# Kernel optimization log

Hardware: AMD Instinct MI355X
Metric: run time of the kernel (lower is better)

## Reference

```python
import jax, jax.numpy as jnp
import numpy as np

NEG_INF = -jnp.inf


def setup_inputs() -> dict:
    key = jax.random.key(0)
    ks = jax.random.split(key, 20)
    B, N, M = 8, 1024, 128
    F_OP, F_MA, F_E, OUT, HID = 64, 64, 16, 64, 128
    inp = {
        "x": jax.random.normal(ks[0], (B, N, F_OP), dtype=jnp.float32),
        "y": jax.random.normal(ks[1], (B, M, F_MA), dtype=jnp.float32),
        "z": jax.random.normal(ks[2], (B, N, M, F_E), dtype=jnp.float32),
        "op_adj_in": jax.random.randint(ks[3], (B, N, N), 0, 2, dtype=jnp.int32),
        "ma_adj_in": jax.random.randint(ks[4], (B, N, N), 0, 2, dtype=jnp.int32),
        "op_ma_adj": jax.random.randint(ks[5], (B, N, M), 0, 2, dtype=jnp.int32),
        # learned parameters
        "weight_op": jax.random.normal(ks[6], (F_OP, OUT), dtype=jnp.float32) * 0.1,
        "weight_ma": jax.random.normal(ks[7], (F_MA, OUT), dtype=jnp.float32) * 0.1,
        "weight_edge": jax.random.normal(ks[8], (F_E, OUT), dtype=jnp.float32) * 0.1,
        "attention_op": jax.random.normal(ks[9], (1, 2 * OUT), dtype=jnp.float32) * 0.1,
        "attention_ma": jax.random.normal(ks[10], (1, 3 * OUT), dtype=jnp.float32) * 0.1,
        "w1": jax.random.normal(ks[11], (2 * OUT, HID), dtype=jnp.float32) * 0.1,
        "b1": jnp.zeros((HID,), dtype=jnp.float32),
        "w2": jax.random.normal(ks[12], (HID, HID), dtype=jnp.float32) * 0.1,
        "b2": jnp.zeros((HID,), dtype=jnp.float32),
        "wo": jax.random.normal(ks[13], (HID, OUT), dtype=jnp.float32) * 0.1,
        "bo": jnp.zeros((OUT,), dtype=jnp.float32),
    }
    return inp


def reference(x, y, z, op_adj_in, ma_adj_in, op_ma_adj,
              weight_op, weight_ma, weight_edge, attention_op, attention_ma,
              w1, b1, w2, b2, wo, bo):
    OUT = weight_op.shape[1]
    h = jnp.einsum('bni,io->bno', x, weight_op)  # [B,N,OUT]
    # all_combinations[b,i,j] = cat(h[b,j], h[b,i]); dot with attention_op splits:
    a1 = attention_op[0, :OUT]
    a2 = attention_op[0, OUT:]
    e_op = (h @ a2)[:, :, None] + (h @ a1)[:, None, :]  # [B,N,N]
    e_op = jax.nn.leaky_relu(e_op, negative_slope=0.01)

    adj = (jnp.swapaxes(op_adj_in, 1, 2) + op_adj_in
           + jnp.swapaxes(ma_adj_in, 1, 2) + ma_adj_in)  # [B,N,N]
    row_mask = jnp.all(op_ma_adj == 0, axis=-1)  # [B,N] ops with no machine link
    adj = jnp.where(row_mask[:, :, None], 1, adj)
    att = jnp.where(adj > 0, e_op, NEG_INF)
    attention_in_op = jax.nn.softmax(att, axis=2)
    h_prime_op = jnp.einsum('bij,bjo->bio', attention_in_op, h)  # [B,N,OUT]

    h_ma = jnp.einsum('bmi,io->bmo', y, weight_ma)  # [B,M,OUT]
    h_edge = jnp.einsum('bnmi,io->bnmo', z, weight_edge)  # [B,N,M,OUT]
    # cat([h_op_i, h_ma_j, h_edge_ij]) @ attention_ma split into three dots
    am1 = attention_ma[0, :OUT]
    am2 = attention_ma[0, OUT:2 * OUT]
    am3 = attention_ma[0, 2 * OUT:]
    e_ma = (h @ am1)[:, :, None] + (h_ma @ am2)[:, None, :] + h_edge @ am3  # [B,N,M]
    e_ma = jax.nn.leaky_relu(e_ma, negative_slope=0.01)

    adj2 = jnp.where(row_mask[:, :, None], 1, op_ma_adj)
    att2 = jnp.where(adj2 > 0, e_ma, NEG_INF)
    attention_in_ma = jax.nn.softmax(att2, axis=2)  # [B,N,M]
    h_ma_edge = h_ma[:, None, :, :] + h_edge  # [B,N,M,OUT]
    h_prime_ma = jnp.einsum('bnm,bnmo->bno', attention_in_ma, h_ma_edge) + h

    h_prime = jnp.concatenate([h_prime_op, h_prime_ma], axis=-1)  # [B,N,2*OUT]
    embed = jax.nn.elu(h_prime @ w1 + b1)
    embed = jax.nn.elu(embed @ w2 + b2)
    embed = embed @ wo + bo
    embed = jnp.where(row_mask[:, :, None], 0.0, embed)
    return embed
```

## Files before the change

kernel.cpp:

```cpp
#include <hip/hip_runtime.h>
#include <math.h>

#define BB 8
#define NN 1024
#define MM 128
#define FOUT 64
#define HIDN 128

#define OFF_H       0
#define OFF_HMA     524288
#define OFF_HA1     589824
#define OFF_HA2     598016
#define OFF_HAM1    606208
#define OFF_HMAAM2  614400
#define OFF_RMASK   615424
#define OFF_WAM3    623616
#define OFF_HPRIME  623632
#define OFF_RDIR    1672208
#define OFF_OPMB    1934352
#define OFF_WT1HI   1967120
#define OFF_WT1LO   1975312
#define OFF_WT2HI   1983504
#define OFF_WT2LO   1991696
#define OFF_WTOHI   1999888
#define OFF_WTOLO   2003984
#define OFF_HTHI    2008080
#define OFF_HTLO    2270224
#define OFF_HMATHI  2532368
#define OFF_HMATLO  2565136

typedef __attribute__((ext_vector_type(8))) short bf16x8;
typedef __attribute__((ext_vector_type(8))) unsigned short u16x8;
typedef __attribute__((ext_vector_type(4))) float f32x4;

__device__ __forceinline__ void splitbf(float v, unsigned short& h, unsigned short& l) {
    unsigned u = __float_as_uint(v);
    unsigned hb = (u + 0x7FFFu + ((u >> 16) & 1u)) >> 16;
    float hf = __uint_as_float(hb << 16);
    float lf = v - hf;
    unsigned ul = __float_as_uint(lf);
    unsigned lb = (ul + 0x7FFFu + ((ul >> 16) & 1u)) >> 16;
    h = (unsigned short)hb; l = (unsigned short)lb;
}

__global__ __launch_bounds__(256) void k1_prep(
    const float* __restrict__ x, const float* __restrict__ y,
    const int* __restrict__ op_ma_adj,
    const int* __restrict__ op_adj, const int* __restrict__ ma_adj,
    const float* __restrict__ w_op, const float* __restrict__ w_ma,
    const float* __restrict__ w_edge,
    const float* __restrict__ att_op, const float* __restrict__ att_ma,
    const float* __restrict__ w1_g, const float* __restrict__ w2_g,
    const float* __restrict__ wo_g,
    float* __restrict__ h, float* __restrict__ h_ma,
    float* __restrict__ ha1, float* __restrict__ ha2, float* __restrict__ ham1,
    float* __restrict__ hmaam2, int* __restrict__ rmask, float* __restrict__ wam3,
    unsigned long long* __restrict__ rowdir, unsigned long long* __restrict__ opmb,
    unsigned short* __restrict__ wt1hi, unsigned short* __restrict__ wt1lo,
    unsigned short* __restrict__ wt2hi, unsigned short* __restrict__ wt2lo,
    unsigned short* __restrict__ wtohi, unsigned short* __restrict__ wtolo,
    unsigned short* __restrict__ hthi, unsigned short* __restrict__ htlo,
    unsigned short* __restrict__ hmathi, unsigned short* __restrict__ hmatlo)
{
    __shared__ float wlds[64 * 64];
    __shared__ unsigned hstage[32 * 64];
    int bid = blockIdx.x;
    int t = threadIdx.x;
    int lane = t & 63;
    int wv = t >> 6;

    if (bid < 256) {
        int b = bid >> 5;
        int n0g = (bid & 31) * 32;
        for (int k = t; k < 4096; k += 256) wlds[k] = w_op[k];
        float a1c = att_op[lane], a2c = att_op[64 + lane], am1c = att_ma[lane];
        __syncthreads();
        #pragma unroll
        for (int p = 0; p < 8; ++p) {
            int row = b * NN + n0g + p * 4 + wv;
            float xv = x[(size_t)row * 64 + lane];
            float acc = 0.f;
            #pragma unroll
            for (int i = 0; i < 64; ++i) {
                float xi = __shfl(xv, i);
                acc += xi * wlds[i * 64 + lane];
            }
            h[(size_t)row * 64 + lane] = acc;
            unsigned short hs, ls;
            splitbf(acc, hs, ls);
            hstage[(p * 4 + wv) * 64 + lane] = (unsigned)hs | ((unsigned)ls << 16);
            float d1 = acc * a1c, d2 = acc * a2c, d3 = acc * am1c;
            #pragma unroll
            for (int m = 32; m; m >>= 1) {
                d1 += __shfl_xor(d1, m);
                d2 += __shfl_xor(d2, m);
                d3 += __shfl_xor(d3, m);
            }
            int v0 = op_ma_adj[(size_t)row * 128 + lane];
            int v1 = op_ma_adj[(size_t)row * 128 + 64 + lane];
            unsigned long long w0 = __ballot(v0 != 0);
            unsigned long long w1 = __ballot(v1 != 0);
            if (lane == 0) {
                ha1[row] = d1; ha2[row] = d2; ham1[row] = d3;
                opmb[row * 2] = w0; opmb[row * 2 + 1] = w1;
                rmask[row] = ((w0 | w1) == 0ULL) ? 1 : 0;
            }
        }
        __syncthreads();
        {
            int plane = t >> 7;
            int q = t & 127;
            int o = q >> 1;
            int hf = q & 1;
            int sh = plane * 16;
            unsigned short* dst = plane ? htlo : hthi;
            u16x8 pk0, pk1;
            #pragma unroll
            for (int k = 0; k < 8; ++k)
                pk0[k] = (unsigned short)((hstage[(hf * 16 + k) * 64 + o] >> sh) & 0xFFFFu);
            #pragma unroll
            for (int k = 0; k < 8; ++k)
                pk1[k] = (unsigned short)((hstage[(hf * 16 + 8 + k) * 64 + o] >> sh) & 0xFFFFu);
            size_t base = ((size_t)(b * 64 + o)) * 1024 + n0g + hf * 16;
            *(u16x8*)&dst[base] = pk0;
            *(u16x8*)&dst[base + 8] = pk1;
        }
    } else if (bid < 288) {
        int bb = (bid - 256) >> 2;
        int m0 = ((bid - 256) & 3) * 32;
        for (int k = t; k < 4096; k += 256) wlds[k] = w_ma[k];
        float am2c = att_ma[64 + lane];
        __syncthreads();
        #pragma unroll
        for (int p = 0; p < 8; ++p) {
            int row = bb * MM + m0 + p * 4 + wv;
            float yv = y[(size_t)row * 64 + lane];
            float acc = 0.f;
            #pragma unroll
            for (int i = 0; i < 64; ++i) {
                float yi = __shfl(yv, i);
                acc += yi * wlds[i * 64 + lane];
            }
            h_ma[(size_t)row * 64 + lane] = acc;
            unsigned short hs, ls;
            splitbf(acc, hs, ls);
            hstage[(p * 4 + wv) * 64 + lane] = (unsigned)hs | ((unsigned)ls << 16);
            float d = acc * am2c;
            #pragma unroll
            for (int m = 32; m; m >>= 1) d += __shfl_xor(d, m);
            if (lane == 0) hmaam2[row] = d;
        }
        __syncthreads();
        {
            int plane = t >> 7;
            int q = t & 127;
            int o = q >> 1;
            int hf = q & 1;
            int sh = plane * 16;
            unsigned short* dst = plane ? hmatlo : hmathi;
            u16x8 pk0, pk1;
            #pragma unroll
            for (int k = 0; k < 8; ++k)
                pk0[k] = (unsigned short)((hstage[(hf * 16 + k) * 64 + o] >> sh) & 0xFFFFu);
            #pragma unroll
            for (int k = 0; k < 8; ++k)
                pk1[k] = (unsigned short)((hstage[(hf * 16 + 8 + k) * 64 + o] >> sh) & 0xFFFFu);
            size_t base = ((size_t)(bb * 64 + o)) * 128 + m0 + hf * 16;
            *(u16x8*)&dst[base] = pk0;
            *(u16x8*)&dst[base + 8] = pk1;
        }
    } else if (bid == 288) {
        if (t < 16) {
            float s = 0.f;
            for (int o = 0; o < 64; ++o) s += w_edge[t * 64 + o] * att_ma[128 + o];
            wam3[t] = s;
        }
    } else if (bid < 2337) {
        unsigned char (*nib)[4][64] = (unsigned char(*)[4][64])wlds;
        int p = bid - 289;
        int b = p >> 8;
        int rg = p & 255;
        int rl = t >> 6;
        int row = rg * 4 + rl;
        const int4* oprow = (const int4*)(op_adj + ((size_t)(b * NN + row)) * NN);
        const int4* marow = (const int4*)(ma_adj + ((size_t)(b * NN + row)) * NN);
        #pragma unroll
        for (int p2 = 0; p2 < 4; ++p2) {
            int4 vo = oprow[p2 * 64 + lane];
            int4 vm = marow[p2 * 64 + lane];
            unsigned nb = ((vo.x | vm.x) ? 1u : 0u) | ((vo.y | vm.y) ? 2u : 0u)
                        | ((vo.z | vm.z) ? 4u : 0u) | ((vo.w | vm.w) ? 8u : 0u);
            nib[rl][p2][lane] = (unsigned char)nb;
        }
        __syncthreads();
        if (t < 64) {
            int arl = t >> 4, q = t & 15;
            const unsigned* nw = (const unsigned*)&nib[arl][q >> 2][(q & 3) * 16];
            unsigned long long w = 0;
            #pragma unroll
            for (int u = 0; u < 4; ++u) {
                unsigned v = nw[u];
                w |= (unsigned long long)(v & 0xFu)         << (16 * u);
                w |= (unsigned long long)((v >> 8) & 0xFu)  << (16 * u + 4);
                w |= (unsigned long long)((v >> 16) & 0xFu) << (16 * u + 8);
                w |= (unsigned long long)((v >> 24) & 0xFu) << (16 * u + 12);
            }
            rowdir[((size_t)(b * NN + rg * 4 + arl)) * 16 + q] = w;
        }
    } else {
        float (*tls)[33] = (float(*)[33])wlds;
        int p = bid - 2337;
        const float* src; unsigned short *dhi, *dlo; int KD, CD, tI, tJ;
        if (p < 16)      { src = w1_g; dhi = wt1hi; dlo = wt1lo; KD = 128; CD = 128; tI = p >> 2; tJ = p & 3; }
        else if (p < 32) { src = w2_g; dhi = wt2hi; dlo = wt2lo; KD = 128; CD = 128; tI = (p-16) >> 2; tJ = (p-16) & 3; }
        else             { src = wo_g; dhi = wtohi; dlo = wtolo; KD = 128; CD = 64;  tI = (p-32) >> 1; tJ = (p-32) & 1; }
        int k0 = tI * 32, c0 = tJ * 32;
        #pragma unroll
        for (int it = 0; it < 4; ++it) {
            int r = (t >> 5) + it * 8;
            int c = t & 31;
            tls[r][c] = src[(size_t)(k0 + r) * CD + c0 + c];
        }
        __syncthreads();
        #pragma unroll
        for (int it = 0; it < 4; ++it) {
            int c = (t >> 5) + it * 8;
            int k = t & 31;
            unsigned short hs, ls;
            splitbf(tls[k][c], hs, ls);
            dhi[(size_t)(c0 + c) * KD + k0 + k] = hs;
            dlo[(size_t)(c0 + c) * KD + k0 + k] = ls;
        }
    }
}

__global__ __launch_bounds__(256) void k2_opatt(
    const unsigned long long* __restrict__ rowdir,
    const unsigned short* __restrict__ hthi,
    const unsigned short* __restrict__ htlo,
    const float* __restrict__ ha1, const float* __restrict__ ha2,
    const int* __restrict__ rmask, float* __restrict__ h_prime)
{
    __shared__ __align__(16) unsigned short Pl[16 * 1024];
    __shared__ float ha1s[1024];
    __shared__ unsigned long long dirw[16][16];
    __shared__ unsigned short trw[1024];
    __shared__ float rdeninv[16];
    int bid = blockIdx.x;
    int b = bid >> 6;
    int i0 = (bid & 63) << 4;
    int t = threadIdx.x;

    {
        int row = t >> 4, w = t & 15;
        dirw[row][w] = rowdir[((size_t)(b * NN + i0 + row)) * 16 + w];
    }
    {
        const char* base = (const char*)rowdir + (size_t)b * NN * 128 + (i0 >> 3);
        #pragma unroll
        for (int jj = 0; jj < 4; ++jj) {
            int j = t + jj * 256;
            trw[j] = *(const unsigned short*)(base + (size_t)j * 128);
        }
    }
    ha1s[t] = ha1[b * NN + t];
    ha1s[t + 256] = ha1[b * NN + t + 256];
    ha1s[t + 512] = ha1[b * NN + t + 512];
    ha1s[t + 768] = ha1[b * NN + t + 768];
    __syncthreads();

    {
        int row = t >> 4, q = t & 15;
        int bn = b * NN + i0 + row;
        float ha2i = ha2[bn];
        unsigned rmf = rmask[bn] ? 1u : 0u;

        float mx = -INFINITY;
        #pragma unroll 8
        for (int jj = 0; jj < 64; ++jj) {
            int j = q + (jj << 4);
            float ev = ha2i + ha1s[j];
            ev = ev > 0.f ? ev : 0.01f * ev;
            unsigned bit = ((unsigned)(dirw[row][jj >> 2] >> (q + ((jj & 3) << 4))) & 1u)
                         | ((unsigned)(trw[j] >> row) & 1u) | rmf;
            if (bit) mx = fmaxf(mx, ev);
        }
        #pragma unroll
        for (int m = 1; m < 16; m <<= 1) mx = fmaxf(mx, __shfl_xor(mx, m));

        float s = 0.f;
        #pragma unroll 4
        for (int jj = 0; jj < 64; ++jj) {
            int j = q + (jj << 4);
            float ev = ha2i + ha1s[j];
            ev = ev > 0.f ? ev : 0.01f * ev;
            unsigned bit = ((unsigned)(dirw[row][jj >> 2] >> (q + ((jj & 3) << 4))) & 1u)
                         | ((unsigned)(trw[j] >> row) & 1u) | rmf;
            float u = bit ? __expf(ev - mx) : 0.f;
            s += u;
            unsigned ub = __float_as_uint(u);
            unsigned short pb = (unsigned short)((ub + 0x7FFFu + ((ub >> 16) & 1u)) >> 16);
            unsigned byteoff = ((unsigned)(row * 2048 + j * 2)) ^ ((unsigned)((row & 7) << 4));
            *(unsigned short*)((char*)Pl + byteoff) = pb;
        }
        #pragma unroll
        for (int m = 1; m < 16; m <<= 1) s += __shfl_xor(s, m);
        if (q == 0) rdeninv[row] = 1.f / s;
    }
    __syncthreads();

    {
        int lane = t & 63, wvv = t >> 6;
        int arow = lane & 15, kg = lane >> 4;
        int col = wvv * 16 + arow;
        const unsigned short* bhp = hthi + ((size_t)(b * 64 + col)) * 1024;
        const unsigned short* blp = htlo + ((size_t)(b * 64 + col)) * 1024;
        f32x4 acc = {0.f, 0.f, 0.f, 0.f};
        #pragma unroll 8
        for (int kst = 0; kst < 32; ++kst) {
            unsigned cc = ((unsigned)(kst * 4 + kg)) ^ ((unsigned)(arow & 7));
            bf16x8 pa = *(const bf16x8*)((char*)Pl + arow * 2048 + cc * 16);
            bf16x8 vh = *(const bf16x8*)&bhp[kst * 32 + kg * 8];
            bf16x8 vl = *(const bf16x8*)&blp[kst * 32 + kg * 8];
            acc = __builtin_amdgcn_mfma_f32_16x16x32_bf16(pa, vh, acc, 0, 0, 0);
            acc = __builtin_amdgcn_mfma_f32_16x16x32_bf16(pa, vl, acc, 0, 0, 0);
        }
        size_t base = (size_t)(b * NN + i0);
        #pragma unroll
        for (int r = 0; r < 4; ++r) {
            int orow = kg * 4 + r;
            float v = acc[r] * rdeninv[orow];
            h_prime[(base + orow) * 128 + col] = v;
        }
    }
}

__global__ __launch_bounds__(256) void k3_maatt(
    const float* __restrict__ z, const unsigned long long* __restrict__ opmb,
    const float* __restrict__ h,
    const unsigned short* __restrict__ hmathi, const unsigned short* __restrict__ hmatlo,
    const float* __restrict__ ham1, const float* __restrict__ hmaam2,
    const int* __restrict__ rmask, const float* __restrict__ wam3,
    const float* __restrict__ w_edge, float* __restrict__ h_prime)
{
    __shared__ __align__(16) unsigned short U_lds[16 * 136];
    __shared__ float wedge_s[1024];
    __shared__ float wam3s[16];
    __shared__ float zsum_s[16][16];
    __shared__ float zpart[4][16];
    __shared__ float redmx[4], redsm[4];
    __shared__ float rdeninv[16];

    int bid = blockIdx.x;
    int b = bid >> 6;
    int n0 = (bid & 63) * 16;
    int t = threadIdx.x;
    int lane = t & 63;
    int wvid = t >> 6;
    int ns = t >> 7;
    int m = t & 127;

    for (int k = t; k < 1024; k += 256) wedge_s[k] = w_edge[k];
    if (t < 16) wam3s[t] = wam3[t];
    __syncthreads();

    float hmam2v = hmaam2[b * MM + m];

    for (int pp = 0; pp < 8; ++pp) {
        int n = n0 + pp * 2 + ns;
        int bn = b * NN + n;

        float zv[16];
        {
            size_t zbase = ((size_t)bn * MM + m) * 16;
            float4 z0 = *(const float4*)(z + zbase);
            float4 z1 = *(const float4*)(z + zbase + 4);
            float4 z2 = *(const float4*)(z + zbase + 8);
            float4 z3 = *(const float4*)(z + zbase + 12);
            zv[0]=z0.x; zv[1]=z0.y; zv[2]=z0.z; zv[3]=z0.w;
            zv[4]=z1.x; zv[5]=z1.y; zv[6]=z1.z; zv[7]=z1.w;
            zv[8]=z2.x; zv[9]=z2.y; zv[10]=z2.z; zv[11]=z2.w;
            zv[12]=z3.x; zv[13]=z3.y; zv[14]=z3.z; zv[15]=z3.w;
        }

        float e = ham1[bn] + hmam2v;
        #pragma unroll
        for (int i = 0; i < 16; ++i) e += zv[i] * wam3s[i];
        e = e > 0.f ? e : 0.01f * e;
        unsigned long long bits = opmb[(size_t)bn * 2 + (m >> 6)];
        int valid = rmask[bn] | (int)((bits >> (m & 63)) & 1ULL);
        e = valid ? e : -INFINITY;

        float mx = e;
        #pragma unroll
        for (int msk = 32; msk; msk >>= 1) mx = fmaxf(mx, __shfl_xor(mx, msk));
        if (lane == 0) redmx[wvid] = mx;
        __syncthreads();
        mx = fmaxf(redmx[ns * 2], redmx[ns * 2 + 1]);
        float uu = __expf(e - mx);

        {
            unsigned ub = __float_as_uint(uu);
            unsigned short pb = (unsigned short)((ub + 0x7FFFu + ((ub >> 16) & 1u)) >> 16);
            U_lds[(pp * 2 + ns) * 136 + m] = pb;
        }

        float sv = uu;
        #pragma unroll
        for (int msk = 32; msk; msk >>= 1) sv += __shfl_xor(sv, msk);
        if (lane == 0) redsm[wvid] = sv;

        #pragma unroll
        for (int i = 0; i < 16; ++i) zv[i] *= uu;
        #pragma unroll
        for (int s2 = 0; s2 < 8; ++s2) {
            float sel = (lane & 1) ? zv[s2] : zv[s2 + 8];
            float got = __shfl_xor(sel, 1);
            zv[s2] = ((lane & 1) ? zv[s2 + 8] : zv[s2]) + got;
        }
        #pragma unroll
        for (int s2 = 0; s2 < 4; ++s2) {
            float sel = (lane & 2) ? zv[s2] : zv[s2 + 4];
            float got = __shfl_xor(sel, 2);
            zv[s2] = ((lane & 2) ? zv[s2 + 4] : zv[s2]) + got;
        }
        #pragma unroll
        for (int s2 = 0; s2 < 2; ++s2) {
            float sel = (lane & 4) ? zv[s2] : zv[s2 + 2];
            float got = __shfl_xor(sel, 4);
            zv[s2] = ((lane & 4) ? zv[s2 + 2] : zv[s2]) + got;
        }
        {
            float sel = (lane & 8) ? zv[0] : zv[1];
            float got = __shfl_xor(sel, 8);
            zv[0] = ((lane & 8) ? zv[1] : zv[0]) + got;
        }
        zv[0] += __shfl_xor(zv[0], 16);
        zv[0] += __shfl_xor(zv[0], 32);
        if (lane < 16) {
            int comp = ((lane & 1) << 3) | ((lane & 2) << 1) | ((lane & 4) >> 1) | ((lane & 8) >> 3);
            zpart[wvid][comp] = zv[0];
        }
        __syncthreads();
        if (t < 32) {
            int ns2 = t >> 4, i = t & 15;
            zsum_s[pp * 2 + ns2][i] = zpart[ns2 * 2][i] + zpart[ns2 * 2 + 1][i];
        }
        if ((t & 127) == 0) rdeninv[pp * 2 + ns] = 1.f / (redsm[ns * 2] + redsm[ns * 2 + 1]);
        __syncthreads();
    }

    {
        int arow = lane & 15, kg = lane >> 4;
        int col = wvid * 16 + arow;
        bf16x8 ua[4];
        #pragma unroll
        for (int ks = 0; ks < 4; ++ks)
            ua[ks] = *(const bf16x8*)&U_lds[arow * 136 + kg * 8 + ks * 32];
        const unsigned short* bhp = hmathi + ((size_t)(b * 64 + col)) * 128 + kg * 8;
        const unsigned short* blp = hmatlo + ((size_t)(b * 64 + col)) * 128 + kg * 8;
        f32x4 acc = {0.f, 0.f, 0.f, 0.f};
        #pragma unroll
        for (int ks = 0; ks < 4; ++ks) {
            bf16x8 bh = *(const bf16x8*)&bhp[ks * 32];
            bf16x8 bl = *(const bf16x8*)&blp[ks * 32];
            acc = __builtin_amdgcn_mfma_f32_16x16x32_bf16(ua[ks], bh, acc, 0, 0, 0);
            acc = __builtin_amdgcn_mfma_f32_16x16x32_bf16(ua[ks], bl, acc, 0, 0, 0);
        }
        #pragma unroll
        for (int r = 0; r < 4; ++r) {
            int row = kg * 4 + r;
            float he = 0.f;
            #pragma unroll
            for (int i = 0; i < 16; ++i) he += zsum_s[row][i] * wedge_s[i * 64 + col];
            int bn = b * NN + n0 + row;
            float val = (acc[r] + he) * rdeninv[row] + h[(size_t)bn * 64 + col];
            h_prime[(size_t)bn * 128 + 64 + col] = val;
        }
    }
}

__global__ __launch_bounds__(256) void k4_mlp(
    const float* __restrict__ hp, const int* __restrict__ rmask,
    const unsigned short* __restrict__ wt1hi, const unsigned short* __restrict__ wt1lo,
    const unsigned short* __restrict__ wt2hi, const unsigned short* __restrict__ wt2lo,
    const unsigned short* __restrict__ wtohi, const unsigned short* __restrict__ wtolo,
    const float* __restrict__ b1, const float* __restrict__ b2,
    const float* __restrict__ bo, float* __restrict__ out)
{
    __shared__ __align__(16) unsigned short Ahi0[16 * 136];
    __shared__ __align__(16) unsigned short Alo0[16 * 136];
    __shared__ __align__(16) unsigned short Ahi1[16 * 136];
    __shared__ __align__(16) unsigned short Alo1[16 * 136];
    __shared__ int rml[16];
    int t = threadIdx.x;
    int lane = t & 63;
    int wv = t >> 6;
    int row0 = blockIdx.x * 16;

    {
        int r = t >> 4;
        int cg = (t & 15) * 8;
        const float* src = hp + (size_t)(row0 + r) * 128 + cg;
        float4 v0 = *(const float4*)src;
        float4 v1 = *(const float4*)(src + 4);
        float xs[8] = {v0.x, v0.y, v0.z, v0.w, v1.x, v1.y, v1.z, v1.w};
        u16x8 hv, lv;
        #pragma unroll
        for (int j = 0; j < 8; ++j) {
            unsigned short hs, ls;
            splitbf(xs[j], hs, ls);
            hv[j] = hs; lv[j] = ls;
        }
        *(u16x8*)&Ahi0[r * 136 + cg] = hv;
        *(u16x8*)&Alo0[r * 136 + cg] = lv;
        if (t < 16) rml[t] = rmask[row0 + t];
    }
    __syncthreads();

    int arow = lane & 15;
    int kg = lane >> 4;
    int aoff = arow * 136 + kg * 8;

    {
        bf16x8 ah[4], al[4];
        #pragma unroll
        for (int ks = 0; ks < 4; ++ks) {
            ah[ks] = *(const bf16x8*)&Ahi0[aoff + ks * 32];
            al[ks] = *(const bf16x8*)&Alo0[aoff + ks * 32];
        }
        #pragma unroll
        for (int q = 0; q < 2; ++q) {
            int ct = wv + q * 4;
            int col = ct * 16 + arow;
            const unsigned short* wh = wt1hi + (size_t)col * 128 + kg * 8;
            const unsigned short* wl = wt1lo + (size_t)col * 128 + kg * 8;
            f32x4 acc = {0.f, 0.f, 0.f, 0.f};
            #pragma unroll
            for (int ks = 0; ks < 4; ++ks) {
                bf16x8 bh = *(const bf16x8*)&wh[ks * 32];
                bf16x8 bl = *(const bf16x8*)&wl[ks * 32];
                acc = __builtin_amdgcn_mfma_f32_16x16x32_bf16(ah[ks], bh, acc, 0, 0, 0);
                acc = __builtin_amdgcn_mfma_f32_16x16x32_bf16(al[ks], bh, acc, 0, 0, 0);
                acc = __builtin_amdgcn_mfma_f32_16x16x32_bf16(ah[ks], bl, acc, 0, 0, 0);
            }
            float bb = b1[col];
            #pragma unroll
            for (int r = 0; r < 4; ++r) {
                int row = kg * 4 + r;
                float v = acc[r] + bb;
                v = v > 0.f ? v : __expf(v) - 1.f;
                unsigned short hs, ls;
                splitbf(v, hs, ls);
                Ahi1[row * 136 + col] = hs;
                Alo1[row * 136 + col] = ls;
            }
        }
    }
    __syncthreads();

    {
        bf16x8 ah[4], al[4];
        #pragma unroll
        for (int ks = 0; ks < 4; ++ks) {
            ah[ks] = *(const bf16x8*)&Ahi1[aoff + ks * 32];
            al[ks] = *(const bf16x8*)&Alo1[aoff + ks * 32];
        }
        #pragma unroll
        for (int q = 0; q < 2; ++q) {
            int ct = wv + q * 4;
            int col = ct * 16 + arow;
            const unsigned short* wh = wt2hi + (size_t)col * 128 + kg * 8;
            const unsigned short* wl = wt2lo + (size_t)col * 128 + kg * 8;
            f32x4 acc = {0.f, 0.f, 0.f, 0.f};
            #pragma unroll
            for (int ks = 0; ks < 4; ++ks) {
                bf16x8 bh = *(const bf16x8*)&wh[ks * 32];
                bf16x8 bl = *(const bf16x8*)&wl[ks * 32];
                acc = __builtin_amdgcn_mfma_f32_16x16x32_bf16(ah[ks], bh, acc, 0, 0, 0);
                acc = __builtin_amdgcn_mfma_f32_16x16x32_bf16(al[ks], bh, acc, 0, 0, 0);
                acc = __builtin_amdgcn_mfma_f32_16x16x32_bf16(ah[ks], bl, acc, 0, 0, 0);
            }
            float bb = b2[col];
            #pragma unroll
            for (int r = 0; r < 4; ++r) {
                int row = kg * 4 + r;
                float v = acc[r] + bb;
                v = v > 0.f ? v : __expf(v) - 1.f;
                unsigned short hs, ls;
                splitbf(v, hs, ls);
                Ahi0[row * 136 + col] = hs;
                Alo0[row * 136 + col] = ls;
            }
        }
    }
    __syncthreads();

    {
        bf16x8 ah[4], al[4];
        #pragma unroll
        for (int ks = 0; ks < 4; ++ks) {
            ah[ks] = *(const bf16x8*)&Ahi0[aoff + ks * 32];
            al[ks] = *(const bf16x8*)&Alo0[aoff + ks * 32];
        }
        int ct = wv;
        int col = ct * 16 + arow;
        const unsigned short* wh = wtohi + (size_t)col * 128 + kg * 8;
        const unsigned short* wl = wtolo + (size_t)col * 128 + kg * 8;
        f32x4 acc = {0.f, 0.f, 0.f, 0.f};
        #pragma unroll
        for (int ks = 0; ks < 4; ++ks) {
            bf16x8 bh = *(const bf16x8*)&wh[ks * 32];
            bf16x8 bl = *(const bf16x8*)&wl[ks * 32];
            acc = __builtin_amdgcn_mfma_f32_16x16x32_bf16(ah[ks], bh, acc, 0, 0, 0);
            acc = __builtin_amdgcn_mfma_f32_16x16x32_bf16(al[ks], bh, acc, 0, 0, 0);
            acc = __builtin_amdgcn_mfma_f32_16x16x32_bf16(ah[ks], bl, acc, 0, 0, 0);
        }
        float bb = bo[col];
        #pragma unroll
        for (int r = 0; r < 4; ++r) {
            int row = kg * 4 + r;
            float v = acc[r] + bb;
            out[(size_t)(row0 + row) * 64 + col] = rml[row] ? 0.f : v;
        }
    }
}

extern "C" void kernel_launch(void* const* d_in, const int* in_sizes, int n_in,
                              void* d_out, int out_size, void* d_ws, size_t ws_size,
                              hipStream_t stream) {
    const float* x      = (const float*)d_in[0];
    const float* y      = (const float*)d_in[1];
    const float* z      = (const float*)d_in[2];
    const int*   op_adj = (const int*)d_in[3];
    const int*   ma_adj = (const int*)d_in[4];
    const int*   opma   = (const int*)d_in[5];
    const float* w_op   = (const float*)d_in[6];
    const float* w_ma   = (const float*)d_in[7];
    const float* w_edge = (const float*)d_in[8];
    const float* att_op = (const float*)d_in[9];
    const float* att_ma = (const float*)d_in[10];
    const float* w1     = (const float*)d_in[11];
    const float* b1     = (const float*)d_in[12];
    const float* w2     = (const float*)d_in[13];
    const float* b2     = (const float*)d_in[14];
    const float* wo     = (const float*)d_in[15];
    const float* bo     = (const float*)d_in[16];
    float* out = (float*)d_out;

    float* ws = (float*)d_ws;
    float* h       = ws + OFF_H;
    float* h_ma    = ws + OFF_HMA;
    float* ha1     = ws + OFF_HA1;
    float* ha2     = ws + OFF_HA2;
    float* ham1    = ws + OFF_HAM1;
    float* hmaam2  = ws + OFF_HMAAM2;
    int*   rmask   = (int*)(ws + OFF_RMASK);
    float* wam3    = ws + OFF_WAM3;
    float* h_prime = ws + OFF_HPRIME;
    unsigned long long* rowdir = (unsigned long long*)(ws + OFF_RDIR);
    unsigned long long* opmb = (unsigned long long*)(ws + OFF_OPMB);
    unsigned short* wt1hi = (unsigned short*)(ws + OFF_WT1HI);
    unsigned short* wt1lo = (unsigned short*)(ws + OFF_WT1LO);
    unsigned short* wt2hi = (unsigned short*)(ws + OFF_WT2HI);
    unsigned short* wt2lo = (unsigned short*)(ws + OFF_WT2LO);
    unsigned short* wtohi = (unsigned short*)(ws + OFF_WTOHI);
    unsigned short* wtolo = (unsigned short*)(ws + OFF_WTOLO);
    unsigned short* hthi  = (unsigned short*)(ws + OFF_HTHI);
    unsigned short* htlo  = (unsigned short*)(ws + OFF_HTLO);
    unsigned short* hmathi = (unsigned short*)(ws + OFF_HMATHI);
    unsigned short* hmatlo = (unsigned short*)(ws + OFF_HMATLO);

    k1_prep<<<256 + 32 + 1 + 2048 + 40, 256, 0, stream>>>(
        x, y, opma, op_adj, ma_adj, w_op, w_ma, w_edge, att_op, att_ma,
        w1, w2, wo,
        h, h_ma, ha1, ha2, ham1, hmaam2, rmask, wam3, rowdir, opmb,
        wt1hi, wt1lo, wt2hi, wt2lo, wtohi, wtolo, hthi, htlo, hmathi, hmatlo);

    k2_opatt<<<512, 256, 0, stream>>>(
        rowdir, hthi, htlo, ha1, ha2, rmask, h_prime);

    k3_maatt<<<512, 256, 0, stream>>>(
        z, opmb, h, hmathi, hmatlo, ham1, hmaam2, rmask, wam3, w_edge, h_prime);

    k4_mlp<<<512, 256, 0, stream>>>(
        h_prime, rmask, wt1hi, wt1lo, wt2hi, wt2lo, wtohi, wtolo,
        b1, b2, bo, out);
}
```

Measured before the change: 97.80 us.

## Add transposed adjacency bitmap and restructure ma-attention to one wave per row

k1 now also writes a transposed 16-bit adjacency mask array (trm), so k2 can load its column-direction mask with two coalesced 32-bit loads per thread instead of strided 2-byte gathers from rowdir. k3 is reorganised so each wavefront handles a whole op row (two machine columns per lane), keeping the softmax max and sum inside the wave and dropping the per-row block barriers and cross-wave shared reductions. This trades extra global writes in k1 and more registers in k3 for fewer syncs and better coalescing.

Measured after the change: 88.38 us. 9.6% less time.

```diff
diff --git a/kernel.cpp b/kernel.cpp
--- a/kernel.cpp
+++ b/kernel.cpp
@@ -28,6 +28,7 @@
 #define OFF_HTLO    2270224
 #define OFF_HMATHI  2532368
 #define OFF_HMATLO  2565136
+#define OFF_TRM     2597904
 
 typedef __attribute__((ext_vector_type(8))) short bf16x8;
 typedef __attribute__((ext_vector_type(8))) unsigned short u16x8;
@@ -41,6 +42,11 @@
     unsigned ul = __float_as_uint(lf);
     unsigned lb = (ul + 0x7FFFu + ((ul >> 16) & 1u)) >> 16;
     h = (unsigned short)hb; l = (unsigned short)lb;
+}
+
+__device__ __forceinline__ unsigned short tobf(float v) {
+    unsigned u = __float_as_uint(v);
+    return (unsigned short)((u + 0x7FFFu + ((u >> 16) & 1u)) >> 16);
 }
 
 __global__ __launch_bounds__(256) void k1_prep(
@@ -56,6 +62,7 @@
     float* __restrict__ ha1, float* __restrict__ ha2, float* __restrict__ ham1,
     float* __restrict__ hmaam2, int* __restrict__ rmask, float* __restrict__ wam3,
     unsigned long long* __restrict__ rowdir, unsigned long long* __restrict__ opmb,
+    unsigned short* __restrict__ trm,
     unsigned short* __restrict__ wt1hi, unsigned short* __restrict__ wt1lo,
     unsigned short* __restrict__ wt2hi, unsigned short* __restrict__ wt2lo,
     unsigned short* __restrict__ wtohi, unsigned short* __restrict__ wtolo,
@@ -121,7 +128,7 @@
             #pragma unroll
             for (int k = 0; k < 8; ++k)
                 pk1[k] = (unsigned short)((hstage[(hf * 16 + 8 + k) * 64 + o] >> sh) & 0xFFFFu);
-            size_t base = ((size_t)(b * 64 + o)) * 1024 + n0g + hf * 16;
+            size_t base = ((size_t)((bid >> 5) * 64 + o)) * 1024 + n0g + hf * 16;
             *(u16x8*)&dst[base] = pk0;
             *(u16x8*)&dst[base + 8] = pk1;
         }
@@ -205,7 +212,13 @@
                 w |= (unsigned long long)((v >> 16) & 0xFu) << (16 * u + 8);
                 w |= (unsigned long long)((v >> 24) & 0xFu) << (16 * u + 12);
             }
-            rowdir[((size_t)(b * NN + rg * 4 + arl)) * 16 + q] = w;
+            int jrow = rg * 4 + arl;
+            rowdir[((size_t)(b * NN + jrow)) * 16 + q] = w;
+            #pragma unroll
+            for (int s = 0; s < 4; ++s) {
+                trm[((size_t)(b * 64 + q * 4 + s)) * 1024 + jrow] =
+                    (unsigned short)((w >> (16 * s)) & 0xFFFFu);
+            }
         }
     } else {
         float (*tls)[33] = (float(*)[33])wlds;
@@ -236,6 +249,7 @@
 
 __global__ __launch_bounds__(256) void k2_opatt(
     const unsigned long long* __restrict__ rowdir,
+    const unsigned short* __restrict__ trm,
     const unsigned short* __restrict__ hthi,
     const unsigned short* __restrict__ htlo,
     const float* __restrict__ ha1, const float* __restrict__ ha2,
@@ -256,12 +270,9 @@
         dirw[row][w] = rowdir[((size_t)(b * NN + i0 + row)) * 16 + w];
     }
     {
-        const char* base = (const char*)rowdir + (size_t)b * NN * 128 + (i0 >> 3);
-        #pragma unroll
-        for (int jj = 0; jj < 4; ++jj) {
-            int j = t + jj * 256;
-            trw[j] = *(const unsigned short*)(base + (size_t)j * 128);
-        }
+        const unsigned* src = (const unsigned*)(trm + ((size_t)(b * 64 + (i0 >> 4))) * 1024);
+        ((unsigned*)trw)[t] = src[t];
+        ((unsigned*)trw)[t + 256] = src[t + 256];
     }
     ha1s[t] = ha1[b * NN + t];
     ha1s[t + 256] = ha1[b * NN + t + 256];
@@ -298,8 +309,7 @@
                          | ((unsigned)(trw[j] >> row) & 1u) | rmf;
             float u = bit ? __expf(ev - mx) : 0.f;
             s += u;
-            unsigned ub = __float_as_uint(u);
-            unsigned short pb = (unsigned short)((ub + 0x7FFFu + ((ub >> 16) & 1u)) >> 16);
+            unsigned short pb = tobf(u);
             unsigned byteoff = ((unsigned)(row * 2048 + j * 2)) ^ ((unsigned)((row & 7) << 4));
             *(unsigned short*)((char*)Pl + byteoff) = pb;
         }
@@ -347,8 +357,6 @@
     __shared__ float wedge_s[1024];
     __shared__ float wam3s[16];
     __shared__ float zsum_s[16][16];
-    __shared__ float zpart[4][16];
-    __shared__ float redmx[4], redsm[4];
     __shared__ float rdeninv[16];
 
     int bid = blockIdx.x;
@@ -356,62 +364,71 @@
     int n0 = (bid & 63) * 16;
     int t = threadIdx.x;
     int lane = t & 63;
-    int wvid = t >> 6;
-    int ns = t >> 7;
-    int m = t & 127;
+    int wv = t >> 6;
 
     for (int k = t; k < 1024; k += 256) wedge_s[k] = w_edge[k];
     if (t < 16) wam3s[t] = wam3[t];
     __syncthreads();
 
-    float hmam2v = hmaam2[b * MM + m];
-
-    for (int pp = 0; pp < 8; ++pp) {
-        int n = n0 + pp * 2 + ns;
-        int bn = b * NN + n;
+    float hm0 = hmaam2[b * MM + lane];
+    float hm1 = hmaam2[b * MM + 64 + lane];
+
+    for (int pp = 0; pp < 4; ++pp) {
+        int nl = pp * 4 + wv;
+        int bn = b * NN + n0 + nl;
+        const float4* zr = (const float4*)(z + (size_t)bn * MM * 16);
+        float4 a0 = zr[lane * 4 + 0];
+        float4 a1 = zr[lane * 4 + 1];
+        float4 a2 = zr[lane * 4 + 2];
+        float4 a3 = zr[lane * 4 + 3];
+        float4 c0 = zr[(lane + 64) * 4 + 0];
+        float4 c1 = zr[(lane + 64) * 4 + 1];
+        float4 c2 = zr[(lane + 64) * 4 + 2];
+        float4 c3 = zr[(lane + 64) * 4 + 3];
+
+        float base = ham1[bn];
+        float e0 = base + hm0;
+        float e1 = base + hm1;
+        e0 += a0.x*wam3s[0] + a0.y*wam3s[1] + a0.z*wam3s[2] + a0.w*wam3s[3]
+            + a1.x*wam3s[4] + a1.y*wam3s[5] + a1.z*wam3s[6] + a1.w*wam3s[7]
+            + a2.x*wam3s[8] + a2.y*wam3s[9] + a2.z*wam3s[10] + a2.w*wam3s[11]
+            + a3.x*wam3s[12] + a3.y*wam3s[13] + a3.z*wam3s[14] + a3.w*wam3s[15];
+        e1 += c0.x*wam3s[0] + c0.y*wam3s[1] + c0.z*wam3s[2] + c0.w*wam3s[3]
+            + c1.x*wam3s[4] + c1.y*wam3s[5] + c1.z*wam3s[6] + c1.w*wam3s[7]
+            + c2.x*wam3s[8] + c2.y*wam3s[9] + c2.z*wam3s[10] + c2.w*wam3s[11]
+            + c3.x*wam3s[12] + c3.y*wam3s[13] + c3.z*wam3s[14] + c3.w*wam3s[15];
+        e0 = e0 > 0.f ? e0 : 0.01f * e0;
+        e1 = e1 > 0.f ? e1 : 0.01f * e1;
+        unsigned long long bits0 = opmb[(size_t)bn * 2];
+        unsigned long long bits1 = opmb[(size_t)bn * 2 + 1];
+        int rm = rmask[bn];
+        int v0 = rm | (int)((bits0 >> lane) & 1ULL);
+        int v1 = rm | (int)((bits1 >> lane) & 1ULL);
+        e0 = v0 ? e0 : -INFINITY;
+        e1 = v1 ? e1 : -INFINITY;
+
+        float mx = fmaxf(e0, e1);
+        #pragma unroll
+        for (int msk = 32; msk; msk >>= 1) mx = fmaxf(mx, __shfl_xor(mx, msk));
+        float u0 = __expf(e0 - mx);
+        float u1 = __expf(e1 - mx);
+        float s = u0 + u1;
+        #pragma unroll
+        for (int msk = 32; msk; msk >>= 1) s += __shfl_xor(s, msk);
+
+        U_lds[nl * 136 + lane] = tobf(u0);
+        U_lds[nl * 136 + 64 + lane] = tobf(u1);
+        if (lane == 0) rdeninv[nl] = 1.f / s;
 
         float zv[16];
-        {
-            size_t zbase = ((size_t)bn * MM + m) * 16;
-            float4 z0 = *(const float4*)(z + zbase);
-            float4 z1 = *(const float4*)(z + zbase + 4);
-            float4 z2 = *(const float4*)(z + zbase + 8);
-            float4 z3 = *(const float4*)(z + zbase + 12);
-            zv[0]=z0.x; zv[1]=z0.y; zv[2]=z0.z; zv[3]=z0.w;
-            zv[4]=z1.x; zv[5]=z1.y; zv[6]=z1.z; zv[7]=z1.w;
-            zv[8]=z2.x; zv[9]=z2.y; zv[10]=z2.z; zv[11]=z2.w;
-            zv[12]=z3.x; zv[13]=z3.y; zv[14]=z3.z; zv[15]=z3.w;
-        }
-
-        float e = ham1[bn] + hmam2v;
-        #pragma unroll
-        for (int i = 0; i < 16; ++i) e += zv[i] * wam3s[i];
-        e = e > 0.f ? e : 0.01f * e;
-        unsigned long long bits = opmb[(size_t)bn * 2 + (m >> 6)];
-        int valid = rmask[bn] | (int)((bits >> (m & 63)) & 1ULL);
-        e = valid ? e : -INFINITY;
-
-        float mx = e;
-        #pragma unroll
-        for (int msk = 32; msk; msk >>= 1) mx = fmaxf(mx, __shfl_xor(mx, msk));
-        if (lane == 0) redmx[wvid] = mx;
-        __syncthreads();
-        mx = fmaxf(redmx[ns * 2], redmx[ns * 2 + 1]);
-        float uu = __expf(e - mx);
-
-        {
-            unsigned ub = __float_as_uint(uu);
-            unsigned short pb = (unsigned short)((ub + 0x7FFFu + ((ub >> 16) & 1u)) >> 16);
-            U_lds[(pp * 2 + ns) * 136 + m] = pb;
-        }
-
-        float sv = uu;
-        #pragma unroll
-        for (int msk = 32; msk; msk >>= 1) sv += __shfl_xor(sv, msk);
-        if (lane == 0) redsm[wvid] = sv;
-
-        #pragma unroll
-        for (int i = 0; i < 16; ++i) zv[i] *= uu;
+        zv[0]=u0*a0.x+u1*c0.x;  zv[1]=u0*a0.y+u1*c0.y;
+        zv[2]=u0*a0.z+u1*c0.z;  zv[3]=u0*a0.w+u1*c0.w;
+        zv[4]=u0*a1.x+u1*c1.x;  zv[5]=u0*a1.y+u1*c1.y;
+        zv[6]=u0*a1.z+u1*c1.z;  zv[7]=u0*a1.w+u1*c1.w;
+        zv[8]=u0*a2.x+u1*c2.x;  zv[9]=u0*a2.y+u1*c2.y;
+        zv[10]=u0*a2.z+u1*c2.z; zv[11]=u0*a2.w+u1*c2.w;
+        zv[12]=u0*a3.x+u1*c3.x; zv[13]=u0*a3.y+u1*c3.y;
+        zv[14]=u0*a3.z+u1*c3.z; zv[15]=u0*a3.w+u1*c3.w;
         #pragma unroll
         for (int s2 = 0; s2 < 8; ++s2) {
             float sel = (lane & 1) ? zv[s2] : zv[s2 + 8];
@@ -439,20 +456,14 @@
         zv[0] += __shfl_xor(zv[0], 32);
         if (lane < 16) {
             int comp = ((lane & 1) << 3) | ((lane & 2) << 1) | ((lane & 4) >> 1) | ((lane & 8) >> 3);
-            zpart[wvid][comp] = zv[0];
-        }
-        __syncthreads();
-        if (t < 32) {
-            int ns2 = t >> 4, i = t & 15;
-            zsum_s[pp * 2 + ns2][i] = zpart[ns2 * 2][i] + zpart[ns2 * 2 + 1][i];
-        }
-        if ((t & 127) == 0) rdeninv[pp * 2 + ns] = 1.f / (redsm[ns * 2] + redsm[ns * 2 + 1]);
-        __syncthreads();
-    }
+            zsum_s[nl][comp] = zv[0];
+        }
+    }
+    __syncthreads();
 
     {
         int arow = lane & 15, kg = lane >> 4;
-        int col = wvid * 16 + arow;
+        int col = wv * 16 + arow;
         bf16x8 ua[4];
         #pragma unroll
         for (int ks = 0; ks < 4; ++ks)
@@ -660,6 +671,7 @@
     float* h_prime = ws + OFF_HPRIME;
     unsigned long long* rowdir = (unsigned long long*)(ws + OFF_RDIR);
     unsigned long long* opmb = (unsigned long long*)(ws + OFF_OPMB);
+    unsigned short* trm   = (unsigned short*)(ws + OFF_TRM);
     unsigned short* wt1hi = (unsigned short*)(ws + OFF_WT1HI);
     unsigned short* wt1lo = (unsigned short*)(ws + OFF_WT1LO);
     unsigned short* wt2hi = (unsigned short*)(ws + OFF_WT2HI);
@@ -674,11 +686,11 @@
     k1_prep<<<256 + 32 + 1 + 2048 + 40, 256, 0, stream>>>(
         x, y, opma, op_adj, ma_adj, w_op, w_ma, w_edge, att_op, att_ma,
         w1, w2, wo,
-        h, h_ma, ha1, ha2, ham1, hmaam2, rmask, wam3, rowdir, opmb,
+        h, h_ma, ha1, ha2, ham1, hmaam2, rmask, wam3, rowdir, opmb, trm,
         wt1hi, wt1lo, wt2hi, wt2lo, wtohi, wtolo, hthi, htlo, hmathi, hmatlo);
 
     k2_opatt<<<512, 256, 0, stream>>>(
-        rowdir, hthi, htlo, ha1, ha2, rmask, h_prime);
+        rowdir, trm, hthi, htlo, ha1, ha2, rmask, h_prime);
 
     k3_maatt<<<512, 256, 0, stream>>>(
         z, opmb, h, hmathi, hmatlo, ham1, hmaam2, rmask, wam3, w_edge, h_prime);
```
